# Performance work log

Measured on AMD Instinct MI355X. Metric: run time of the kernel, lower is better.

The kernel has to match this reference:

```python
import jax, jax.numpy as jnp
import numpy as np

EPS = 1e-5
N_HEAD = 12
N_LAYER = 12
D = 768
VOCAB = 50257
SEQ = 1024


def layer_norm(x, w, b):
    m = jnp.mean(x, axis=-1, keepdims=True)
    v = jnp.mean(jnp.square(x - m), axis=-1, keepdims=True)
    return (x - m) * jax.lax.rsqrt(v + EPS) * w + b


def setup_inputs() -> dict:
    key = jax.random.key(0)
    ks = jax.random.split(key, 8)
    s = 0.02  # gpt2 init scale
    return {
        "input_ids": jax.random.randint(ks[0], (SEQ,), 0, VOCAB, dtype=jnp.int64 if jax.config.jax_enable_x64 else jnp.int32),
        "wte": jax.random.normal(ks[1], (VOCAB, D), jnp.float32) * s,
        "wpe": jax.random.normal(ks[2], (SEQ, D), jnp.float32) * s,
        "ln1_w": jnp.ones((N_LAYER, D), jnp.float32),
        "ln1_b": jnp.zeros((N_LAYER, D), jnp.float32),
        "qkv_w": jax.random.normal(ks[3], (N_LAYER, D, 3 * D), jnp.float32) * s,
        "qkv_b": jnp.zeros((N_LAYER, 3 * D), jnp.float32),
        "out_w": jax.random.normal(ks[4], (N_LAYER, D, D), jnp.float32) * s,
        "out_b": jnp.zeros((N_LAYER, D), jnp.float32),
        "ln2_w": jnp.ones((N_LAYER, D), jnp.float32),
        "ln2_b": jnp.zeros((N_LAYER, D), jnp.float32),
        "up_w": jax.random.normal(ks[5], (N_LAYER, D, 4 * D), jnp.float32) * s,
        "up_b": jnp.zeros((N_LAYER, 4 * D), jnp.float32),
        "down_w": jax.random.normal(ks[6], (N_LAYER, 4 * D, D), jnp.float32) * s,
        "down_b": jnp.zeros((N_LAYER, D), jnp.float32),
        "lnf_w": jnp.ones((D,), jnp.float32),
        "lnf_b": jnp.zeros((D,), jnp.float32),
    }


def _attention(x, qkv_w, qkv_b, out_w, out_b, causal_mask):
    S = x.shape[0]
    d = D // N_HEAD
    qkv = x @ qkv_w + qkv_b                  # [S, 3D]
    q, k, v = jnp.split(qkv, 3, axis=-1)     # each [S, D]
    q = q.reshape(S, N_HEAD, d)
    k = k.reshape(S, N_HEAD, d)
    v = v.reshape(S, N_HEAD, d)
    scores = jnp.einsum('shd,thd->hst', q, k) / np.sqrt(d).astype(np.float32)
    scores = jnp.where(causal_mask, scores, jnp.finfo(scores.dtype).min)
    p = jax.nn.softmax(scores, axis=-1)      # [H, S, S]
    o = jnp.einsum('hst,thd->shd', p, v).reshape(S, D)
    return o @ out_w + out_b


def reference(input_ids, wte, wpe, ln1_w, ln1_b, qkv_w, qkv_b, out_w, out_b,
              ln2_w, ln2_b, up_w, up_b, down_w, down_b, lnf_w, lnf_b):
    S = input_ids.shape[0]
    h0 = wte[input_ids] + wpe[jnp.arange(S)]        # [S, D]
    causal_mask = jnp.tril(jnp.ones((S, S), bool))

    layer_params = (ln1_w, ln1_b, qkv_w, qkv_b, out_w, out_b,
                    ln2_w, ln2_b, up_w, up_b, down_w, down_b)

    def step(x, p):
        l1w, l1b, qw, qb, ow, ob, l2w, l2b, uw, ub, dw, db = p
        x = x + _attention(layer_norm(x, l1w, l1b), qw, qb, ow, ob, causal_mask)
        x = x + (jax.nn.gelu(layer_norm(x, l2w, l2b) @ uw + ub, approximate=True) @ dw + db)
        return x, x

    h, ys = jax.lax.scan(step, h0, layer_params)
    layers_output = jnp.concatenate([h0[None], ys], axis=0)   # [L+1, S, D]
    return layer_norm(h, lnf_w, lnf_b), layers_output
```

## Files before the change

kernel.cpp:

```cpp
#include <hip/hip_runtime.h>

typedef __bf16 bf16_t;
typedef __bf16 bf16x8 __attribute__((ext_vector_type(8)));
typedef __bf16 bf16x4 __attribute__((ext_vector_type(4)));
typedef float f32x4 __attribute__((ext_vector_type(4)));

#define MFMA16(a, b, c) __builtin_amdgcn_mfma_f32_16x16x32_bf16(a, b, c, 0, 0, 0)

__device__ __forceinline__ f32x4 zero4() {
    f32x4 z = {0.f, 0.f, 0.f, 0.f};
    return z;
}

__device__ __forceinline__ float gelu_f(float v) {
    float u = 0.7978845608028654f * (v + 0.044715f * v * v * v);
    float e = __expf(2.0f * u);
    float th = 1.0f - 2.0f / (e + 1.0f);
    return 0.5f * v * (1.0f + th);
}

__device__ __forceinline__ void gload16(const bf16_t* g, bf16_t* l) {
    __builtin_amdgcn_global_load_lds((const __attribute__((address_space(1))) void*)g,
                                     (__attribute__((address_space(3))) void*)l, 16, 0, 0);
}

__global__ __launch_bounds__(256) void embed_kernel(const int* __restrict__ ids,
                                                    const float* __restrict__ wte,
                                                    const float* __restrict__ wpe,
                                                    float* __restrict__ x,
                                                    float* __restrict__ out0) {
    const int s = blockIdx.x;
    const int id = ids[s];
    const size_t base = (size_t)s * 768;
#pragma unroll
    for (int r = 0; r < 3; ++r) {
        int d = threadIdx.x + r * 256;
        float v = wte[(size_t)id * 768 + d] + wpe[base + d];
        x[base + d] = v;
        out0[base + d] = v;
    }
}

template <bool BF16OUT>
__global__ __launch_bounds__(256) void ln_kernel(const float* __restrict__ x,
                                                 const float* __restrict__ w,
                                                 const float* __restrict__ b,
                                                 void* __restrict__ outp) {
    const int row = blockIdx.x;
    const int t = threadIdx.x;
    const float* xr = x + (size_t)row * 768;
    float v0 = xr[t], v1 = xr[t + 256], v2 = xr[t + 512];
    float s = v0 + v1 + v2;
    float q = v0 * v0 + v1 * v1 + v2 * v2;
#pragma unroll
    for (int off = 32; off >= 1; off >>= 1) {
        s += __shfl_xor(s, off);
        q += __shfl_xor(q, off);
    }
    __shared__ float sh_s[4], sh_q[4];
    if ((t & 63) == 0) {
        sh_s[t >> 6] = s;
        sh_q[t >> 6] = q;
    }
    __syncthreads();
    s = sh_s[0] + sh_s[1] + sh_s[2] + sh_s[3];
    q = sh_q[0] + sh_q[1] + sh_q[2] + sh_q[3];
    const float mean = s * (1.0f / 768.0f);
    const float var = q * (1.0f / 768.0f) - mean * mean;
    const float rstd = rsqrtf(var + 1e-5f);
    float vv[3] = {v0, v1, v2};
#pragma unroll
    for (int r = 0; r < 3; ++r) {
        int d = t + r * 256;
        float y = (vv[r] - mean) * rstd * w[d] + b[d];
        if (BF16OUT)
            ((bf16_t*)outp)[(size_t)row * 768 + d] = (bf16_t)y;
        else
            ((float*)outp)[(size_t)row * 768 + d] = y;
    }
}

template <bool FINAL>
__global__ __launch_bounds__(256) void ln_reduce(const float* __restrict__ p0,
                                                 const float* __restrict__ p1,
                                                 const float* __restrict__ db,
                                                 float* __restrict__ x,
                                                 float* __restrict__ slice,
                                                 void* __restrict__ lnout,
                                                 const float* __restrict__ w,
                                                 const float* __restrict__ b) {
    const int row = blockIdx.x;
    const int t = threadIdx.x;
    const size_t base = (size_t)row * 768;
    float vv[3];
#pragma unroll
    for (int r = 0; r < 3; ++r) {
        int d = t + r * 256;
        float v = x[base + d] + p0[base + d] + p1[base + d] + db[d];
        vv[r] = v;
        x[base + d] = v;
        slice[base + d] = v;
    }
    float s = vv[0] + vv[1] + vv[2];
    float q = vv[0] * vv[0] + vv[1] * vv[1] + vv[2] * vv[2];
#pragma unroll
    for (int off = 32; off >= 1; off >>= 1) {
        s += __shfl_xor(s, off);
        q += __shfl_xor(q, off);
    }
    __shared__ float sh_s[4], sh_q[4];
    if ((t & 63) == 0) {
        sh_s[t >> 6] = s;
        sh_q[t >> 6] = q;
    }
    __syncthreads();
    s = sh_s[0] + sh_s[1] + sh_s[2] + sh_s[3];
    q = sh_q[0] + sh_q[1] + sh_q[2] + sh_q[3];
    const float mean = s * (1.0f / 768.0f);
    const float var = q * (1.0f / 768.0f) - mean * mean;
    const float rstd = rsqrtf(var + 1e-5f);
#pragma unroll
    for (int r = 0; r < 3; ++r) {
        int d = t + r * 256;
        float y = (vv[r] - mean) * rstd * w[d] + b[d];
        if (FINAL)
            ((float*)lnout)[base + d] = y;
        else
            ((bf16_t*)lnout)[base + d] = (bf16_t)y;
    }
}

__global__ __launch_bounds__(256) void transpose_cvt(const float* __restrict__ src0,
                                                     bf16_t* __restrict__ dst0, int K, int N) {
    const int l = blockIdx.z;
    const float* src = src0 + (size_t)l * K * N;
    bf16_t* dst = dst0 + (size_t)l * N * K;
    const int n0 = blockIdx.x * 32;
    const int k0 = blockIdx.y * 32;
    __shared__ float tile[32][36];
    const int t = threadIdx.x;
    const int r = t >> 3, c4 = (t & 7) * 4;
    const float4 v = *(const float4*)&src[(size_t)(k0 + r) * N + n0 + c4];
    tile[r][c4 + 0] = v.x;
    tile[r][c4 + 1] = v.y;
    tile[r][c4 + 2] = v.z;
    tile[r][c4 + 3] = v.w;
    __syncthreads();
    bf16x4 o;
    o[0] = (bf16_t)tile[c4 + 0][r];
    o[1] = (bf16_t)tile[c4 + 1][r];
    o[2] = (bf16_t)tile[c4 + 2][r];
    o[3] = (bf16_t)tile[c4 + 3][r];
    *(bf16x4*)&dst[(size_t)(n0 + r) * K + k0 + c4] = o;
}

template <int BM, int BN, bool GELU, bool RES, bool VT>
__global__ __launch_bounds__(256) void gemm3(const bf16_t* __restrict__ A,
                                             const bf16_t* __restrict__ BT,
                                             const float* __restrict__ bias,
                                             const float* __restrict__ res,
                                             float* __restrict__ outF,
                                             bf16_t* __restrict__ outB,
                                             bf16_t* __restrict__ vt, int N, int LDK,
                                             int KLEN) {
    constexpr int MW = BM / 32, NW = BN / 32;
    constexpr int TILE = (BM + BN) * 64;
    constexpr int LOADS = (BM + BN) / 32;
    __shared__ __align__(16) bf16_t lds[3 * TILE];
    const int tid = threadIdx.x;
    const int lane = tid & 63, wv = tid >> 6, wm = wv >> 1, wn = wv & 1;
    const int lr = lane & 15, lg = lane >> 4;
    const int m0 = blockIdx.x * BM, n0 = blockIdx.y * BN;
    const bf16_t* Ap = A + (size_t)m0 * LDK + (size_t)blockIdx.z * KLEN;
    const bf16_t* Bp = BT + (size_t)n0 * LDK + (size_t)blockIdx.z * KLEN;

    f32x4 acc[MW][NW];
#pragma unroll
    for (int i = 0; i < MW; ++i)
#pragma unroll
        for (int j = 0; j < NW; ++j) acc[i][j] = zero4();

    const int KT = KLEN >> 6;

    auto stage = [&](int buf, int kt) {
        bf16_t* Ad = lds + buf * TILE;
        bf16_t* Bd = Ad + BM * 64;
#pragma unroll
        for (int i = 0; i < BM / 32; ++i) {
            int v = i * 256 + tid;
            int row = v >> 3, cg = v & 7;
            gload16(Ap + (size_t)row * LDK + kt * 64 + ((cg ^ (row & 7)) << 3), Ad + v * 8);
        }
#pragma unroll
        for (int i = 0; i < BN / 32; ++i) {
            int v = i * 256 + tid;
            int row = v >> 3, cg = v & 7;
            gload16(Bp + (size_t)row * LDK + kt * 64 + ((cg ^ (row & 7)) << 3), Bd + v * 8);
        }
    };

    stage(0, 0);
    stage(1, 1);
    int buf = 0;
    for (int kt = 0; kt < KT; ++kt) {
        if (kt + 1 < KT) {
            if constexpr (LOADS == 4)
                asm volatile("s_waitcnt vmcnt(4)" ::: "memory");
            else
                asm volatile("s_waitcnt vmcnt(3)" ::: "memory");
        } else {
            asm volatile("s_waitcnt vmcnt(0)" ::: "memory");
        }
        __builtin_amdgcn_s_barrier();
        if (kt + 2 < KT) stage((kt + 2) % 3, kt + 2);
        const bf16_t* Ab = lds + buf * TILE;
        const bf16_t* Bb = Ab + BM * 64;
        __builtin_amdgcn_s_setprio(1);
#pragma unroll
        for (int c = 0; c < 2; ++c) {
            bf16x8 af[MW], bfr[NW];
#pragma unroll
            for (int i = 0; i < MW; ++i) {
                int row = wm * (BM / 2) + i * 16 + lr;
                af[i] = *(const bf16x8*)&Ab[row * 64 + ((c * 32 + lg * 8) ^ ((row & 7) << 3))];
            }
#pragma unroll
            for (int j = 0; j < NW; ++j) {
                int row = wn * (BN / 2) + j * 16 + lr;
                bfr[j] = *(const bf16x8*)&Bb[row * 64 + ((c * 32 + lg * 8) ^ ((row & 7) << 3))];
            }
#pragma unroll
            for (int i = 0; i < MW; ++i)
#pragma unroll
                for (int j = 0; j < NW; ++j) acc[i][j] = MFMA16(af[i], bfr[j], acc[i][j]);
        }
        __builtin_amdgcn_s_setprio(0);
        buf = (buf + 1) % 3;
    }

    float* o1 = outF ? outF + (size_t)blockIdx.z * ((size_t)1024 * N) : nullptr;
#pragma unroll
    for (int i = 0; i < MW; ++i) {
#pragma unroll
        for (int j = 0; j < NW; ++j) {
            const int col = n0 + wn * (BN / 2) + j * 16 + lr;
            const float bc = bias ? bias[col] : 0.f;
            float vr[4];
#pragma unroll
            for (int ii = 0; ii < 4; ++ii) {
                const int rrow = m0 + wm * (BM / 2) + i * 16 + lg * 4 + ii;
                float v = acc[i][j][ii] + bc;
                if (GELU) v = gelu_f(v);
                if (RES) v += res[(size_t)rrow * N + col];
                if (o1) o1[(size_t)rrow * N + col] = v;
                if (outB) outB[(size_t)rrow * N + col] = (bf16_t)v;
                vr[ii] = v;
            }
            if (VT && col >= 1536) {
                const int rrow0 = m0 + wm * (BM / 2) + i * 16 + lg * 4;
                bf16x4 o;
#pragma unroll
                for (int ii = 0; ii < 4; ++ii) o[ii] = (bf16_t)vr[ii];
                *(bf16x4*)&vt[(size_t)(col - 1536) * 1024 + rrow0] = o;
            }
        }
    }
}

__global__ __launch_bounds__(256) void attn4_kernel(const bf16_t* __restrict__ qkv,
                                                    const bf16_t* __restrict__ vt,
                                                    bf16_t* __restrict__ out) {
    const int qb = 31 - blockIdx.x;
    const int h = blockIdx.y;
    const int tid = threadIdx.x;
    const int w = tid >> 6, lane = tid & 63;
    const int lr = lane & 15, lg = lane >> 4;
    const int qsub = w & 1, ks = w >> 1;
    const int q0 = qb * 32;
    const int qr0 = q0 + qsub * 16;
    const int NT = (q0 >> 6) + 1;

    __shared__ __align__(16) bf16_t Ksh[2][64 * 64];
    __shared__ __align__(16) bf16_t Vsh[2][64 * 64];
    __shared__ bf16_t Ps[4][16][72];
    __shared__ float Osh[2][16][64];
    __shared__ float mlsh[2][2][16];

    bf16x8 aq[2];
    {
        const size_t qoff = (size_t)(qr0 + lr) * 2304 + h * 64;
#pragma unroll
        for (int dt = 0; dt < 2; ++dt) {
            bf16x8 v = *(const bf16x8*)&qkv[qoff + dt * 32 + lg * 8];
#pragma unroll
            for (int i = 0; i < 8; ++i) v[i] = (bf16_t)((float)v[i] * 0.125f);
            aq[dt] = v;
        }
    }

    f32x4 oacc[4];
#pragma unroll
    for (int i = 0; i < 4; ++i) oacc[i] = zero4();
    float mrun[4], lrun[4];
#pragma unroll
    for (int i = 0; i < 4; ++i) {
        mrun[i] = -3.0e38f;
        lrun[i] = 0.f;
    }

    const int st = tid >> 7, tt = tid & 127;
    const int rounds = (NT + 1) >> 1;

    for (int rr = 0; rr < rounds; ++rr) {
        const int skb = 2 * rr + st;
        if (skb < NT) {
            const int k0s = skb * 64;
#pragma unroll
            for (int i = 0; i < 4; ++i) {
                int v = i * 128 + tt;
                int row = v >> 3, cg = v & 7;
                gload16(qkv + (size_t)(k0s + row) * 2304 + 768 + h * 64 +
                            ((cg ^ (row & 7)) << 3),
                        &Ksh[st][v * 8]);
            }
#pragma unroll
            for (int i = 0; i < 4; ++i) {
                int v = i * 128 + tt;
                int row = v >> 3, cg = v & 7;
                gload16(vt + (size_t)(h * 64 + row) * 1024 + k0s + ((cg ^ (row & 7)) << 3),
                        &Vsh[st][v * 8]);
            }
        }
        __syncthreads();

        const int kb = 2 * rr + ks;
        if (kb < NT) {
            const int k0 = kb * 64;
            f32x4 sacc[4];
#pragma unroll
            for (int i = 0; i < 4; ++i) sacc[i] = zero4();
            __builtin_amdgcn_s_setprio(1);
#pragma unroll
            for (int kt = 0; kt < 4; ++kt) {
                const int row = kt * 16 + lr;
#pragma unroll
                for (int dt = 0; dt < 2; ++dt) {
                    bf16x8 bk = *(const bf16x8*)&Ksh[ks][row * 64 +
                                                        ((dt * 32 + lg * 8) ^ ((row & 7) << 3))];
                    sacc[kt] = MFMA16(aq[dt], bk, sacc[kt]);
                }
            }
            __builtin_amdgcn_s_setprio(0);

            if (kb == NT - 1) {
#pragma unroll
                for (int kt = 0; kt < 4; ++kt)
#pragma unroll
                    for (int i = 0; i < 4; ++i)
                        if (k0 + kt * 16 + lr > qr0 + lg * 4 + i) sacc[kt][i] = -3.0e38f;
            }

#pragma unroll
            for (int i = 0; i < 4; ++i) {
                float rmax = fmaxf(fmaxf(sacc[0][i], sacc[1][i]), fmaxf(sacc[2][i], sacc[3][i]));
                rmax = fmaxf(rmax, __shfl_xor(rmax, 1));
                rmax = fmaxf(rmax, __shfl_xor(rmax, 2));
                rmax = fmaxf(rmax, __shfl_xor(rmax, 4));
                rmax = fmaxf(rmax, __shfl_xor(rmax, 8));
                const float mnew = fmaxf(mrun[i], rmax);
                const float sf = __expf(mrun[i] - mnew);
                mrun[i] = mnew;
                float rsum = 0.f;
#pragma unroll
                for (int kt = 0; kt < 4; ++kt) {
                    float p = __expf(sacc[kt][i] - mnew);
                    rsum += p;
                    Ps[w][lg * 4 + i][kt * 16 + lr] = (bf16_t)p;
                }
                rsum += __shfl_xor(rsum, 1);
                rsum += __shfl_xor(rsum, 2);
                rsum += __shfl_xor(rsum, 4);
                rsum += __shfl_xor(rsum, 8);
                lrun[i] = lrun[i] * sf + rsum;
#pragma unroll
                for (int ot = 0; ot < 4; ++ot) oacc[ot][i] *= sf;
            }

            bf16x8 pa0 = *(const bf16x8*)&Ps[w][lr][lg * 8];
            bf16x8 pa1 = *(const bf16x8*)&Ps[w][lr][32 + lg * 8];
            __builtin_amdgcn_s_setprio(1);
#pragma unroll
            for (int ot = 0; ot < 4; ++ot) {
                const int row = ot * 16 + lr;
                bf16x8 bv0 = *(const bf16x8*)&Vsh[ks][row * 64 +
                                                      ((lg * 8) ^ ((row & 7) << 3))];
                bf16x8 bv1 = *(const bf16x8*)&Vsh[ks][row * 64 +
                                                      ((32 + lg * 8) ^ ((row & 7) << 3))];
                oacc[ot] = MFMA16(pa0, bv0, oacc[ot]);
                oacc[ot] = MFMA16(pa1, bv1, oacc[ot]);
            }
            __builtin_amdgcn_s_setprio(0);
        }
        __syncthreads();
    }

    if (ks == 1) {
        if (lr == 0) {
#pragma unroll
            for (int i = 0; i < 4; ++i) {
                mlsh[qsub][0][lg * 4 + i] = mrun[i];
                mlsh[qsub][1][lg * 4 + i] = lrun[i];
            }
        }
#pragma unroll
        for (int ot = 0; ot < 4; ++ot)
#pragma unroll
            for (int i = 0; i < 4; ++i) Osh[qsub][lg * 4 + i][ot * 16 + lr] = oacc[ot][i];
    }
    __syncthreads();
    if (ks == 0) {
#pragma unroll
        for (int ot = 0; ot < 4; ++ot)
#pragma unroll
            for (int i = 0; i < 4; ++i) {
                const int row = lg * 4 + i;
                const float m1 = mlsh[qsub][0][row], l1 = mlsh[qsub][1][row];
                const float mm = fmaxf(mrun[i], m1);
                const float fa = __expf(mrun[i] - mm), fb = __expf(m1 - mm);
                const float ll = lrun[i] * fa + l1 * fb;
                const float v = (oacc[ot][i] * fa + Osh[qsub][row][ot * 16 + lr] * fb) / ll;
                out[(size_t)(qr0 + row) * 768 + h * 64 + ot * 16 + lr] = (bf16_t)v;
            }
    }
}

extern "C" void kernel_launch(void* const* d_in, const int* in_sizes, int n_in, void* d_out,
                              int out_size, void* d_ws, size_t ws_size, hipStream_t stream) {
    const int* ids = (const int*)d_in[0];
    const float* wte = (const float*)d_in[1];
    const float* wpe = (const float*)d_in[2];
    const float* ln1_w = (const float*)d_in[3];
    const float* ln1_b = (const float*)d_in[4];
    const float* qkv_w = (const float*)d_in[5];
    const float* qkv_b = (const float*)d_in[6];
    const float* out_w = (const float*)d_in[7];
    const float* out_b = (const float*)d_in[8];
    const float* ln2_w = (const float*)d_in[9];
    const float* ln2_b = (const float*)d_in[10];
    const float* up_w = (const float*)d_in[11];
    const float* up_b = (const float*)d_in[12];
    const float* down_w = (const float*)d_in[13];
    const float* down_b = (const float*)d_in[14];
    const float* lnf_w = (const float*)d_in[15];
    const float* lnf_b = (const float*)d_in[16];

    char* ws = (char*)d_ws;
    float* x = (float*)(ws + 0);
    bf16_t* a_bf = (bf16_t*)(ws + 3145728);
    bf16_t* qkv_bf = (bf16_t*)(ws + 4718592);
    bf16_t* attn_bf = (bf16_t*)(ws + 9437184);
    bf16_t* u_bf = (bf16_t*)(ws + 11010048);
    bf16_t* vt = (bf16_t*)(ws + 11010048);
    float* p0 = (float*)(ws + 4718592);
    float* p1 = (float*)(ws + 7864320);
    bf16_t* wqkv_t = (bf16_t*)(ws + 17301504);
    bf16_t* wout_t = (bf16_t*)(ws + 59768832);
    bf16_t* wup_t = (bf16_t*)(ws + 73924608);
    bf16_t* wdown_t = (bf16_t*)(ws + 130547712);

    float* outF = (float*)d_out;
    const size_t SD = (size_t)1024 * 768;
    float* out_layers = outF + SD;

    transpose_cvt<<<dim3(72, 24, 12), 256, 0, stream>>>(qkv_w, wqkv_t, 768, 2304);
    transpose_cvt<<<dim3(24, 24, 12), 256, 0, stream>>>(out_w, wout_t, 768, 768);
    transpose_cvt<<<dim3(96, 24, 12), 256, 0, stream>>>(up_w, wup_t, 768, 3072);
    transpose_cvt<<<dim3(24, 96, 12), 256, 0, stream>>>(down_w, wdown_t, 3072, 768);

    embed_kernel<<<1024, 256, 0, stream>>>(ids, wte, wpe, x, out_layers);

    for (int l = 0; l < 12; ++l) {
        const size_t l768 = (size_t)l * 768;
        if (l == 0)
            ln_kernel<true><<<1024, 256, 0, stream>>>(x, ln1_w, ln1_b, a_bf);
        else
            ln_reduce<false><<<1024, 256, 0, stream>>>(p0, p1, down_b + (l - 1) * 768, x,
                                                       out_layers + (size_t)l * SD, a_bf,
                                                       ln1_w + l768, ln1_b + l768);
        gemm3<64, 64, false, false, true><<<dim3(16, 36), 256, 0, stream>>>(
            a_bf, wqkv_t + (size_t)l * 2304 * 768, qkv_b + (size_t)l * 2304, nullptr, nullptr,
            qkv_bf, vt, 2304, 768, 768);
        attn4_kernel<<<dim3(32, 12), 256, 0, stream>>>(qkv_bf, vt, attn_bf);
        gemm3<64, 64, false, true, false><<<dim3(16, 12), 256, 0, stream>>>(
            attn_bf, wout_t + (size_t)l * 768 * 768, out_b + l768, x, x, nullptr, nullptr, 768,
            768, 768);
        ln_kernel<true><<<1024, 256, 0, stream>>>(x, ln2_w + l768, ln2_b + l768, a_bf);
        gemm3<64, 64, true, false, false><<<dim3(16, 48), 256, 0, stream>>>(
            a_bf, wup_t + (size_t)l * 3072 * 768, up_b + (size_t)l * 3072, nullptr, nullptr,
            u_bf, nullptr, 3072, 768, 768);
        gemm3<64, 64, false, false, false><<<dim3(16, 12, 2), 256, 0, stream>>>(
            u_bf, wdown_t + (size_t)l * 768 * 3072, nullptr, nullptr, p0, nullptr, nullptr, 768,
            3072, 1536);
    }
    ln_reduce<true><<<1024, 256, 0, stream>>>(p0, p1, down_b + 11 * 768, x,
                                              out_layers + 12 * SD, outF, lnf_w, lnf_b);
}
```

Baseline: 1.085 ms.

## Fuse layernorm into GEMM A-operand loading and drop split-K down projection

Layernorm is folded into the QKV and up-projection GEMMs. Each block computes per-row mean and rstd from the fp32 residual, then normalises and converts A tiles to bf16 in registers before writing them to LDS. The down projection drops its two-way split-K and partial buffers for a single 64x32-tile GEMM that adds bias and residual and writes the layer output slice directly, which removes the ln_reduce kernels. This cuts launches and intermediate traffic, but every N-block recomputes the row statistics and A tiles now go through registers instead of direct-to-LDS loads.

```diff
diff --git a/kernel.cpp b/kernel.cpp
--- a/kernel.cpp
+++ b/kernel.cpp
@@ -41,11 +41,10 @@
     }
 }
 
-template <bool BF16OUT>
 __global__ __launch_bounds__(256) void ln_kernel(const float* __restrict__ x,
                                                  const float* __restrict__ w,
                                                  const float* __restrict__ b,
-                                                 void* __restrict__ outp) {
+                                                 float* __restrict__ outp) {
     const int row = blockIdx.x;
     const int t = threadIdx.x;
     const float* xr = x + (size_t)row * 768;
@@ -72,61 +71,7 @@
 #pragma unroll
     for (int r = 0; r < 3; ++r) {
         int d = t + r * 256;
-        float y = (vv[r] - mean) * rstd * w[d] + b[d];
-        if (BF16OUT)
-            ((bf16_t*)outp)[(size_t)row * 768 + d] = (bf16_t)y;
-        else
-            ((float*)outp)[(size_t)row * 768 + d] = y;
-    }
-}
-
-template <bool FINAL>
-__global__ __launch_bounds__(256) void ln_reduce(const float* __restrict__ p0,
-                                                 const float* __restrict__ p1,
-                                                 const float* __restrict__ db,
-                                                 float* __restrict__ x,
-                                                 float* __restrict__ slice,
-                                                 void* __restrict__ lnout,
-                                                 const float* __restrict__ w,
-                                                 const float* __restrict__ b) {
-    const int row = blockIdx.x;
-    const int t = threadIdx.x;
-    const size_t base = (size_t)row * 768;
-    float vv[3];
-#pragma unroll
-    for (int r = 0; r < 3; ++r) {
-        int d = t + r * 256;
-        float v = x[base + d] + p0[base + d] + p1[base + d] + db[d];
-        vv[r] = v;
-        x[base + d] = v;
-        slice[base + d] = v;
-    }
-    float s = vv[0] + vv[1] + vv[2];
-    float q = vv[0] * vv[0] + vv[1] * vv[1] + vv[2] * vv[2];
-#pragma unroll
-    for (int off = 32; off >= 1; off >>= 1) {
-        s += __shfl_xor(s, off);
-        q += __shfl_xor(q, off);
-    }
-    __shared__ float sh_s[4], sh_q[4];
-    if ((t & 63) == 0) {
-        sh_s[t >> 6] = s;
-        sh_q[t >> 6] = q;
-    }
-    __syncthreads();
-    s = sh_s[0] + sh_s[1] + sh_s[2] + sh_s[3];
-    q = sh_q[0] + sh_q[1] + sh_q[2] + sh_q[3];
-    const float mean = s * (1.0f / 768.0f);
-    const float var = q * (1.0f / 768.0f) - mean * mean;
-    const float rstd = rsqrtf(var + 1e-5f);
-#pragma unroll
-    for (int r = 0; r < 3; ++r) {
-        int d = t + r * 256;
-        float y = (vv[r] - mean) * rstd * w[d] + b[d];
-        if (FINAL)
-            ((float*)lnout)[base + d] = y;
-        else
-            ((bf16_t*)lnout)[base + d] = (bf16_t)y;
+        outp[(size_t)row * 768 + d] = (vv[r] - mean) * rstd * w[d] + b[d];
     }
 }
 
@@ -154,12 +99,16 @@
     *(bf16x4*)&dst[(size_t)(n0 + r) * K + k0 + c4] = o;
 }
 
-template <int BM, int BN, bool GELU, bool RES, bool VT>
+template <int BM, int BN, bool GELU, bool RES, bool VT, bool LNA, bool SLICE>
 __global__ __launch_bounds__(256) void gemm3(const bf16_t* __restrict__ A,
+                                             const float* __restrict__ Af32,
                                              const bf16_t* __restrict__ BT,
                                              const float* __restrict__ bias,
                                              const float* __restrict__ res,
+                                             const float* __restrict__ lnw,
+                                             const float* __restrict__ lnb,
                                              float* __restrict__ outF,
+                                             float* __restrict__ outF2,
                                              bf16_t* __restrict__ outB,
                                              bf16_t* __restrict__ vt, int N, int LDK,
                                              int KLEN) {
@@ -167,6 +116,8 @@
     constexpr int TILE = (BM + BN) * 64;
     constexpr int LOADS = (BM + BN) / 32;
     __shared__ __align__(16) bf16_t lds[3 * TILE];
+    __shared__ bf16_t wls[2 * 768];
+    __shared__ float mls[128];
     const int tid = threadIdx.x;
     const int lane = tid & 63, wv = tid >> 6, wm = wv >> 1, wn = wv & 1;
     const int lr = lane & 15, lg = lane >> 4;
@@ -182,37 +133,57 @@
 
     const int KT = KLEN >> 6;
 
-    auto stage = [&](int buf, int kt) {
+    auto stageB = [&](int buf, int kt) {
+        bf16_t* Bd = lds + buf * TILE + BM * 64;
+#pragma unroll
+        for (int i = 0; i < BN / 32; ++i) {
+            int v = i * 256 + tid;
+            int row = v >> 3, cg = v & 7;
+            gload16(Bp + (size_t)row * LDK + kt * 64 + ((cg ^ (row & 7)) << 3), Bd + v * 8);
+        }
+    };
+    auto stageA = [&](int buf, int kt) {
         bf16_t* Ad = lds + buf * TILE;
-        bf16_t* Bd = Ad + BM * 64;
 #pragma unroll
         for (int i = 0; i < BM / 32; ++i) {
             int v = i * 256 + tid;
             int row = v >> 3, cg = v & 7;
             gload16(Ap + (size_t)row * LDK + kt * 64 + ((cg ^ (row & 7)) << 3), Ad + v * 8);
         }
-#pragma unroll
-        for (int i = 0; i < BN / 32; ++i) {
-            int v = i * 256 + tid;
+    };
+    auto a_issue = [&](int kt, float4* regs) {
+#pragma unroll
+        for (int s2 = 0; s2 < 2; ++s2) {
+            int v = s2 * 256 + tid;
             int row = v >> 3, cg = v & 7;
-            gload16(Bp + (size_t)row * LDK + kt * 64 + ((cg ^ (row & 7)) << 3), Bd + v * 8);
+            int c8 = cg ^ (row & 7);
+            const float* src = Af32 + (size_t)(m0 + row) * 768 + kt * 64 + c8 * 8;
+            regs[s2 * 2 + 0] = *(const float4*)src;
+            regs[s2 * 2 + 1] = *(const float4*)(src + 4);
         }
     };
-
-    stage(0, 0);
-    stage(1, 1);
-    int buf = 0;
-    for (int kt = 0; kt < KT; ++kt) {
-        if (kt + 1 < KT) {
-            if constexpr (LOADS == 4)
-                asm volatile("s_waitcnt vmcnt(4)" ::: "memory");
-            else
-                asm volatile("s_waitcnt vmcnt(3)" ::: "memory");
-        } else {
-            asm volatile("s_waitcnt vmcnt(0)" ::: "memory");
-        }
-        __builtin_amdgcn_s_barrier();
-        if (kt + 2 < KT) stage((kt + 2) % 3, kt + 2);
+    auto a_transform = [&](int buf, int kt, const float4* regs) {
+        bf16_t* Ad = lds + buf * TILE;
+#pragma unroll
+        for (int s2 = 0; s2 < 2; ++s2) {
+            int v = s2 * 256 + tid;
+            int row = v >> 3, cg = v & 7;
+            int c8 = cg ^ (row & 7);
+            const float mean = mls[row * 2], rstd = mls[row * 2 + 1];
+            const int cb = kt * 64 + c8 * 8;
+            bf16x8 wv8 = *(const bf16x8*)&wls[cb];
+            bf16x8 bv8 = *(const bf16x8*)&wls[768 + cb];
+            bf16x8 o;
+#pragma unroll
+            for (int jj = 0; jj < 8; ++jj) {
+                float xv = ((const float*)&regs[s2 * 2])[jj];
+                o[jj] = (bf16_t)((xv - mean) * rstd * (float)wv8[jj] + (float)bv8[jj]);
+            }
+            *(bf16x8*)&Ad[v * 8] = o;
+        }
+    };
+
+    auto compute = [&](int buf) {
         const bf16_t* Ab = lds + buf * TILE;
         const bf16_t* Bb = Ab + BM * 64;
         __builtin_amdgcn_s_setprio(1);
@@ -235,7 +206,93 @@
                 for (int j = 0; j < NW; ++j) acc[i][j] = MFMA16(af[i], bfr[j], acc[i][j]);
         }
         __builtin_amdgcn_s_setprio(0);
-        buf = (buf + 1) % 3;
+    };
+
+    if constexpr (LNA) {
+        {
+            const int srow = tid >> 2, sseg = tid & 3;
+            const float* xr = Af32 + (size_t)(m0 + srow) * 768 + sseg * 192;
+            float s = 0.f, q = 0.f;
+#pragma unroll 8
+            for (int j = 0; j < 48; ++j) {
+                float4 v4 = *(const float4*)(xr + j * 4);
+                s += v4.x + v4.y + v4.z + v4.w;
+                q += v4.x * v4.x + v4.y * v4.y + v4.z * v4.z + v4.w * v4.w;
+            }
+            s += __shfl_xor(s, 1);
+            s += __shfl_xor(s, 2);
+            q += __shfl_xor(q, 1);
+            q += __shfl_xor(q, 2);
+            if (sseg == 0) {
+                const float mean = s * (1.0f / 768.0f);
+                const float var = q * (1.0f / 768.0f) - mean * mean;
+                mls[srow * 2] = mean;
+                mls[srow * 2 + 1] = rsqrtf(var + 1e-5f);
+            }
+            if (tid < 192) {
+                float4 wv = *(const float4*)&lnw[tid * 4];
+                float4 bv = *(const float4*)&lnb[tid * 4];
+                bf16x4 wo, bo;
+                wo[0] = (bf16_t)wv.x; wo[1] = (bf16_t)wv.y; wo[2] = (bf16_t)wv.z; wo[3] = (bf16_t)wv.w;
+                bo[0] = (bf16_t)bv.x; bo[1] = (bf16_t)bv.y; bo[2] = (bf16_t)bv.z; bo[3] = (bf16_t)bv.w;
+                *(bf16x4*)&wls[tid * 4] = wo;
+                *(bf16x4*)&wls[768 + tid * 4] = bo;
+            }
+        }
+        __syncthreads();
+
+        float4 ar0[4], ar1[4];
+        a_issue(0, ar0);
+        stageB(0, 0);
+        a_issue(1, ar1);
+        stageB(1, 1);
+        asm volatile("s_waitcnt vmcnt(8)" ::: "memory");
+        a_transform(0, 0, ar0);
+        asm volatile("s_waitcnt vmcnt(2)" ::: "memory");
+        a_transform(1, 1, ar1);
+
+        int buf = 0;
+        float4 ar[4];
+        for (int kt = 0; kt < KT; ++kt) {
+            if (kt + 1 < KT)
+                asm volatile("s_waitcnt vmcnt(2) lgkmcnt(0)" ::: "memory");
+            else
+                asm volatile("s_waitcnt vmcnt(0) lgkmcnt(0)" ::: "memory");
+            __builtin_amdgcn_s_barrier();
+            if (kt + 2 < KT) {
+                a_issue(kt + 2, ar);
+                stageB((kt + 2) % 3, kt + 2);
+            }
+            compute(buf);
+            if (kt + 2 < KT) {
+                asm volatile("s_waitcnt vmcnt(2)" ::: "memory");
+                a_transform((kt + 2) % 3, kt + 2, ar);
+            }
+            buf = (buf + 1) % 3;
+        }
+    } else {
+        stageA(0, 0);
+        stageB(0, 0);
+        stageA(1, 1);
+        stageB(1, 1);
+        int buf = 0;
+        for (int kt = 0; kt < KT; ++kt) {
+            if (kt + 1 < KT) {
+                if constexpr (LOADS == 4)
+                    asm volatile("s_waitcnt vmcnt(4)" ::: "memory");
+                else
+                    asm volatile("s_waitcnt vmcnt(3)" ::: "memory");
+            } else {
+                asm volatile("s_waitcnt vmcnt(0)" ::: "memory");
+            }
+            __builtin_amdgcn_s_barrier();
+            if (kt + 2 < KT) {
+                stageA((kt + 2) % 3, kt + 2);
+                stageB((kt + 2) % 3, kt + 2);
+            }
+            compute(buf);
+            buf = (buf + 1) % 3;
+        }
     }
 
     float* o1 = outF ? outF + (size_t)blockIdx.z * ((size_t)1024 * N) : nullptr;
@@ -253,6 +310,7 @@
                 if (GELU) v = gelu_f(v);
                 if (RES) v += res[(size_t)rrow * N + col];
                 if (o1) o1[(size_t)rrow * N + col] = v;
+                if (SLICE) outF2[(size_t)rrow * N + col] = v;
                 if (outB) outB[(size_t)rrow * N + col] = (bf16_t)v;
                 vr[ii] = v;
             }
@@ -392,10 +450,9 @@
 #pragma unroll
             for (int ot = 0; ot < 4; ++ot) {
                 const int row = ot * 16 + lr;
-                bf16x8 bv0 = *(const bf16x8*)&Vsh[ks][row * 64 +
-                                                      ((lg * 8) ^ ((row & 7) << 3))];
-                bf16x8 bv1 = *(const bf16x8*)&Vsh[ks][row * 64 +
-                                                      ((32 + lg * 8) ^ ((row & 7) << 3))];
+                bf16x8 bv0 = *(const bf16x8*)&Vsh[ks][row * 64 + ((lg * 8) ^ ((row & 7) << 3))];
+                bf16x8 bv1 =
+                    *(const bf16x8*)&Vsh[ks][row * 64 + ((32 + lg * 8) ^ ((row & 7) << 3))];
                 oacc[ot] = MFMA16(pa0, bv0, oacc[ot]);
                 oacc[ot] = MFMA16(pa1, bv1, oacc[ot]);
             }
@@ -456,13 +513,10 @@
 
     char* ws = (char*)d_ws;
     float* x = (float*)(ws + 0);
-    bf16_t* a_bf = (bf16_t*)(ws + 3145728);
-    bf16_t* qkv_bf = (bf16_t*)(ws + 4718592);
-    bf16_t* attn_bf = (bf16_t*)(ws + 9437184);
-    bf16_t* u_bf = (bf16_t*)(ws + 11010048);
-    bf16_t* vt = (bf16_t*)(ws + 11010048);
-    float* p0 = (float*)(ws + 4718592);
-    float* p1 = (float*)(ws + 7864320);
+    bf16_t* qkv_bf = (bf16_t*)(ws + 3145728);
+    bf16_t* attn_bf = (bf16_t*)(ws + 7864320);
+    bf16_t* u_bf = (bf16_t*)(ws + 9437184);
+    bf16_t* vt = (bf16_t*)(ws + 9437184);
     bf16_t* wqkv_t = (bf16_t*)(ws + 17301504);
     bf16_t* wout_t = (bf16_t*)(ws + 59768832);
     bf16_t* wup_t = (bf16_t*)(ws + 73924608);
@@ -481,27 +535,19 @@
 
     for (int l = 0; l < 12; ++l) {
         const size_t l768 = (size_t)l * 768;
-        if (l == 0)
-            ln_kernel<true><<<1024, 256, 0, stream>>>(x, ln1_w, ln1_b, a_bf);
-        else
-            ln_reduce<false><<<1024, 256, 0, stream>>>(p0, p1, down_b + (l - 1) * 768, x,
-                                                       out_layers + (size_t)l * SD, a_bf,
-                                                       ln1_w + l768, ln1_b + l768);
-        gemm3<64, 64, false, false, true><<<dim3(16, 36), 256, 0, stream>>>(
-            a_bf, wqkv_t + (size_t)l * 2304 * 768, qkv_b + (size_t)l * 2304, nullptr, nullptr,
-            qkv_bf, vt, 2304, 768, 768);
+        gemm3<64, 64, false, false, true, true, false><<<dim3(16, 36), 256, 0, stream>>>(
+            nullptr, x, wqkv_t + (size_t)l * 2304 * 768, qkv_b + (size_t)l * 2304, nullptr,
+            ln1_w + l768, ln1_b + l768, nullptr, nullptr, qkv_bf, vt, 2304, 768, 768);
         attn4_kernel<<<dim3(32, 12), 256, 0, stream>>>(qkv_bf, vt, attn_bf);
-        gemm3<64, 64, false, true, false><<<dim3(16, 12), 256, 0, stream>>>(
-            attn_bf, wout_t + (size_t)l * 768 * 768, out_b + l768, x, x, nullptr, nullptr, 768,
-            768, 768);
-        ln_kernel<true><<<1024, 256, 0, stream>>>(x, ln2_w + l768, ln2_b + l768, a_bf);
-        gemm3<64, 64, true, false, false><<<dim3(16, 48), 256, 0, stream>>>(
-            a_bf, wup_t + (size_t)l * 3072 * 768, up_b + (size_t)l * 3072, nullptr, nullptr,
-            u_bf, nullptr, 3072, 768, 768);
-        gemm3<64, 64, false, false, false><<<dim3(16, 12, 2), 256, 0, stream>>>(
-            u_bf, wdown_t + (size_t)l * 768 * 3072, nullptr, nullptr, p0, nullptr, nullptr, 768,
-            3072, 1536);
-    }
-    ln_reduce<true><<<1024, 256, 0, stream>>>(p0, p1, down_b + 11 * 768, x,
-                                              out_layers + 12 * SD, outF, lnf_w, lnf_b);
-}
+        gemm3<64, 64, false, true, false, false, false><<<dim3(16, 12), 256, 0, stream>>>(
+            attn_bf, nullptr, wout_t + (size_t)l * 768 * 768, out_b + l768, x, nullptr,
+            nullptr, x, nullptr, nullptr, nullptr, 768, 768, 768);
+        gemm3<64, 64, true, false, false, true, false><<<dim3(16, 48), 256, 0, stream>>>(
+            nullptr, x, wup_t + (size_t)l * 3072 * 768, up_b + (size_t)l * 3072, nullptr,
+            ln2_w + l768, ln2_b + l768, nullptr, nullptr, u_bf, nullptr, 3072, 768, 768);
+        gemm3<64, 32, false, true, false, false, true><<<dim3(16, 24), 256, 0, stream>>>(
+            u_bf, nullptr, wdown_t + (size_t)l * 768 * 3072, down_b + l768, x, nullptr,
+            nullptr, x, out_layers + (size_t)(l + 1) * SD, nullptr, nullptr, 768, 3072, 3072);
+    }
+    ln_kernel<<<1024, 256, 0, stream>>>(x, lnf_w, lnf_b, outF);
+}
```

Measured after the change: 1.611 ms. 48.4% more time.

## Replace split-K down projection with full-K GEMM fusing bias and residual

Applied to the files above, without the earlier changes.

The down-projection GEMM no longer splits K into two partial outputs that a separate ln_reduce kernel sums. It now runs the full K=3072 with 64x32 tiles, adding bias and residual in its epilogue, writing x and the per-layer output slice directly. LN1 becomes a plain ln_kernel, which removes the partial-sum buffers and their extra global traffic. In exchange each block runs a longer K loop over a 384-block grid, and an extra standalone LN launch replaces the fused reduce+LN.

```diff
diff --git a/kernel.cpp b/kernel.cpp
--- a/kernel.cpp
+++ b/kernel.cpp
@@ -77,56 +77,6 @@
             ((bf16_t*)outp)[(size_t)row * 768 + d] = (bf16_t)y;
         else
             ((float*)outp)[(size_t)row * 768 + d] = y;
-    }
-}
-
-template <bool FINAL>
-__global__ __launch_bounds__(256) void ln_reduce(const float* __restrict__ p0,
-                                                 const float* __restrict__ p1,
-                                                 const float* __restrict__ db,
-                                                 float* __restrict__ x,
-                                                 float* __restrict__ slice,
-                                                 void* __restrict__ lnout,
-                                                 const float* __restrict__ w,
-                                                 const float* __restrict__ b) {
-    const int row = blockIdx.x;
-    const int t = threadIdx.x;
-    const size_t base = (size_t)row * 768;
-    float vv[3];
-#pragma unroll
-    for (int r = 0; r < 3; ++r) {
-        int d = t + r * 256;
-        float v = x[base + d] + p0[base + d] + p1[base + d] + db[d];
-        vv[r] = v;
-        x[base + d] = v;
-        slice[base + d] = v;
-    }
-    float s = vv[0] + vv[1] + vv[2];
-    float q = vv[0] * vv[0] + vv[1] * vv[1] + vv[2] * vv[2];
-#pragma unroll
-    for (int off = 32; off >= 1; off >>= 1) {
-        s += __shfl_xor(s, off);
-        q += __shfl_xor(q, off);
-    }
-    __shared__ float sh_s[4], sh_q[4];
-    if ((t & 63) == 0) {
-        sh_s[t >> 6] = s;
-        sh_q[t >> 6] = q;
-    }
-    __syncthreads();
-    s = sh_s[0] + sh_s[1] + sh_s[2] + sh_s[3];
-    q = sh_q[0] + sh_q[1] + sh_q[2] + sh_q[3];
-    const float mean = s * (1.0f / 768.0f);
-    const float var = q * (1.0f / 768.0f) - mean * mean;
-    const float rstd = rsqrtf(var + 1e-5f);
-#pragma unroll
-    for (int r = 0; r < 3; ++r) {
-        int d = t + r * 256;
-        float y = (vv[r] - mean) * rstd * w[d] + b[d];
-        if (FINAL)
-            ((float*)lnout)[base + d] = y;
-        else
-            ((bf16_t*)lnout)[base + d] = (bf16_t)y;
     }
 }
 
@@ -160,6 +110,7 @@
                                              const float* __restrict__ bias,
                                              const float* __restrict__ res,
                                              float* __restrict__ outF,
+                                             float* __restrict__ outF2,
                                              bf16_t* __restrict__ outB,
                                              bf16_t* __restrict__ vt, int N, int LDK,
                                              int KLEN) {
@@ -253,6 +204,7 @@
                 if (GELU) v = gelu_f(v);
                 if (RES) v += res[(size_t)rrow * N + col];
                 if (o1) o1[(size_t)rrow * N + col] = v;
+                if (outF2) outF2[(size_t)rrow * N + col] = v;
                 if (outB) outB[(size_t)rrow * N + col] = (bf16_t)v;
                 vr[ii] = v;
             }
@@ -392,10 +344,9 @@
 #pragma unroll
             for (int ot = 0; ot < 4; ++ot) {
                 const int row = ot * 16 + lr;
-                bf16x8 bv0 = *(const bf16x8*)&Vsh[ks][row * 64 +
-                                                      ((lg * 8) ^ ((row & 7) << 3))];
-                bf16x8 bv1 = *(const bf16x8*)&Vsh[ks][row * 64 +
-                                                      ((32 + lg * 8) ^ ((row & 7) << 3))];
+                bf16x8 bv0 = *(const bf16x8*)&Vsh[ks][row * 64 + ((lg * 8) ^ ((row & 7) << 3))];
+                bf16x8 bv1 =
+                    *(const bf16x8*)&Vsh[ks][row * 64 + ((32 + lg * 8) ^ ((row & 7) << 3))];
                 oacc[ot] = MFMA16(pa0, bv0, oacc[ot]);
                 oacc[ot] = MFMA16(pa1, bv1, oacc[ot]);
             }
@@ -461,8 +412,6 @@
     bf16_t* attn_bf = (bf16_t*)(ws + 9437184);
     bf16_t* u_bf = (bf16_t*)(ws + 11010048);
     bf16_t* vt = (bf16_t*)(ws + 11010048);
-    float* p0 = (float*)(ws + 4718592);
-    float* p1 = (float*)(ws + 7864320);
     bf16_t* wqkv_t = (bf16_t*)(ws + 17301504);
     bf16_t* wout_t = (bf16_t*)(ws + 59768832);
     bf16_t* wup_t = (bf16_t*)(ws + 73924608);
@@ -481,27 +430,21 @@
 
     for (int l = 0; l < 12; ++l) {
         const size_t l768 = (size_t)l * 768;
-        if (l == 0)
-            ln_kernel<true><<<1024, 256, 0, stream>>>(x, ln1_w, ln1_b, a_bf);
-        else
-            ln_reduce<false><<<1024, 256, 0, stream>>>(p0, p1, down_b + (l - 1) * 768, x,
-                                                       out_layers + (size_t)l * SD, a_bf,
-                                                       ln1_w + l768, ln1_b + l768);
+        ln_kernel<true><<<1024, 256, 0, stream>>>(x, ln1_w + l768, ln1_b + l768, a_bf);
         gemm3<64, 64, false, false, true><<<dim3(16, 36), 256, 0, stream>>>(
             a_bf, wqkv_t + (size_t)l * 2304 * 768, qkv_b + (size_t)l * 2304, nullptr, nullptr,
-            qkv_bf, vt, 2304, 768, 768);
+            nullptr, qkv_bf, vt, 2304, 768, 768);
         attn4_kernel<<<dim3(32, 12), 256, 0, stream>>>(qkv_bf, vt, attn_bf);
         gemm3<64, 64, false, true, false><<<dim3(16, 12), 256, 0, stream>>>(
-            attn_bf, wout_t + (size_t)l * 768 * 768, out_b + l768, x, x, nullptr, nullptr, 768,
-            768, 768);
+            attn_bf, wout_t + (size_t)l * 768 * 768, out_b + l768, x, x, nullptr, nullptr,
+            nullptr, 768, 768, 768);
         ln_kernel<true><<<1024, 256, 0, stream>>>(x, ln2_w + l768, ln2_b + l768, a_bf);
         gemm3<64, 64, true, false, false><<<dim3(16, 48), 256, 0, stream>>>(
             a_bf, wup_t + (size_t)l * 3072 * 768, up_b + (size_t)l * 3072, nullptr, nullptr,
-            u_bf, nullptr, 3072, 768, 768);
-        gemm3<64, 64, false, false, false><<<dim3(16, 12, 2), 256, 0, stream>>>(
-            u_bf, wdown_t + (size_t)l * 768 * 3072, nullptr, nullptr, p0, nullptr, nullptr, 768,
-            3072, 1536);
-    }
-    ln_reduce<true><<<1024, 256, 0, stream>>>(p0, p1, down_b + 11 * 768, x,
-                                              out_layers + 12 * SD, outF, lnf_w, lnf_b);
-}
+            nullptr, u_bf, nullptr, 3072, 768, 768);
+        gemm3<64, 32, false, true, false><<<dim3(16, 24), 256, 0, stream>>>(
+            u_bf, wdown_t + (size_t)l * 768 * 3072, down_b + l768, x, x,
+            out_layers + (size_t)(l + 1) * SD, nullptr, nullptr, 768, 3072, 3072);
+    }
+    ln_kernel<false><<<1024, 256, 0, stream>>>(x, lnf_w, lnf_b, outF);
+}
```

Result: slower. 1.144 ms (+5.4%).
